# Kernel optimization log

Hardware: AMD Instinct MI355X
Metric: run time of the kernel (lower is better)

Reference implementation:

```python
import jax, jax.numpy as jnp
import numpy as np

N_NODES = 50000
N_EDGES = 500000
F_IN = 128
HID = 128
HEADS = 1
N_CLASSES = 5
NEG_SLOPE = 0.2   # PyG GATv2Conv default leaky_relu slope
BN_EPS = 1e-5


def setup_inputs() -> dict:
    key = jax.random.key(0)
    ks = jax.random.split(key, 16)
    d = {
        "x": jax.random.normal(ks[0], (N_NODES, F_IN), jnp.float32),
        "edge_index": jax.random.randint(ks[1], (2, N_EDGES), 0, N_NODES, jnp.int64),
        # GATv2Conv params (lin_l / lin_r with bias, attention vector, output bias)
        "Wl": jax.random.normal(ks[2], (F_IN, HEADS * HID), jnp.float32) * 0.05,
        "bl": jax.random.normal(ks[3], (HEADS * HID,), jnp.float32) * 0.05,
        "Wr": jax.random.normal(ks[4], (F_IN, HEADS * HID), jnp.float32) * 0.05,
        "br": jax.random.normal(ks[5], (HEADS * HID,), jnp.float32) * 0.05,
        "att": jax.random.normal(ks[6], (HEADS, HID), jnp.float32) * 0.05,
        "bias1": jax.random.normal(ks[7], (HID,), jnp.float32) * 0.05,
        # BatchNorm (eval mode: running stats + affine)
        "bn_gamma": jax.random.normal(ks[8], (HID,), jnp.float32) * 0.1 + 1.0,
        "bn_beta": jax.random.normal(ks[9], (HID,), jnp.float32) * 0.1,
        "bn_mean": jax.random.normal(ks[10], (HID,), jnp.float32) * 0.1,
        "bn_var": jax.random.uniform(ks[11], (HID,), jnp.float32, 0.5, 1.5),
        # classifier
        "Wc": jax.random.normal(ks[12], (HID, N_CLASSES), jnp.float32) * 0.05,
        "bc": jax.random.normal(ks[13], (N_CLASSES,), jnp.float32) * 0.05,
    }
    return d


def reference(x, edge_index, Wl, bl, Wr, br, att, bias1,
              bn_gamma, bn_beta, bn_mean, bn_var, Wc, bc):
    n = x.shape[0]
    heads, d = att.shape
    # PyG GATv2Conv default add_self_loops=True
    loops = jnp.arange(n, dtype=edge_index.dtype)
    src = jnp.concatenate([edge_index[0], loops])  # message source j
    dst = jnp.concatenate([edge_index[1], loops])  # aggregation target i

    xl = (x @ Wl + bl).reshape(n, heads, d)  # lin_l -> x_j side
    xr = (x @ Wr + br).reshape(n, heads, d)  # lin_r -> x_i side

    # per-edge GATv2 attention logits: a^T leaky_relu(x_j + x_i)
    e = jax.nn.leaky_relu(xl[src] + xr[dst], NEG_SLOPE)       # [E+N, H, D]
    logits = jnp.einsum('ehd,hd->eh', e, att)                 # [E+N, H]

    # segment softmax over incoming edges of each target node
    m = jax.ops.segment_max(logits, dst, num_segments=n)      # [N, H]
    a = jnp.exp(logits - m[dst])
    denom = jax.ops.segment_sum(a, dst, num_segments=n)
    a = a / denom[dst]                                        # [E+N, H]

    # weighted scatter-add of source features (dropout inactive at eval)
    out = jax.ops.segment_sum(xl[src] * a[:, :, None], dst, num_segments=n)  # [N,H,D]
    out = out.mean(axis=1) + bias1  # concat=False -> average heads, then bias

    # BatchNorm (eval: running stats)
    h = (out - bn_mean) * jax.lax.rsqrt(bn_var + BN_EPS) * bn_gamma + bn_beta

    # global_mean_pool with batch=None -> single graph
    g = h.mean(axis=0, keepdims=True)                         # [1, HID]
    return jax.nn.softmax(g @ Wc + bc, axis=1)                # [1, n_classes]
```

## Files before the change

### kernel.cpp

```cpp
#include <hip/hip_runtime.h>
#include <hip/hip_bf16.h>

typedef __attribute__((ext_vector_type(8))) short short8v;
typedef __attribute__((ext_vector_type(4))) float f32x4;
typedef __attribute__((ext_vector_type(2))) float v2f;

__device__ __forceinline__ unsigned short f2b(float f) {
    union { float f; unsigned int u; } v; v.f = f;
    unsigned int r = (v.u + 0x7fffu + ((v.u >> 16) & 1u)) >> 16;
    return (unsigned short)r;
}
__device__ __forceinline__ unsigned int pack2(float lo, float hi) {
    return (unsigned int)f2b(lo) | ((unsigned int)f2b(hi) << 16);
}
__device__ __forceinline__ void unpk_fp8x4(unsigned int u, float* o) {
    v2f lo = __builtin_amdgcn_cvt_pk_f32_fp8(u, false);
    v2f hi = __builtin_amdgcn_cvt_pk_f32_fp8(u, true);
    o[0] = lo[0]; o[1] = lo[1]; o[2] = hi[0]; o[3] = hi[1];
}

__global__ __launch_bounds__(256) void prep(
    const float* __restrict__ Wl, const float* __restrict__ bl,
    const float* __restrict__ Wr, const float* __restrict__ br,
    unsigned short* __restrict__ Whf, float* __restrict__ bh,
    float* __restrict__ zbuf, int nz)
{
    const int idx    = blockIdx.x * 256 + threadIdx.x;
    const int stride = gridDim.x * 256;

    for (int i = idx; i < 32768; i += stride) {
        int j   = i & 7;
        int l   = (i >> 3) & 63;
        int nfg = (i >> 9) & 15;
        int ks  = i >> 13;
        int k = ks * 32 + (l >> 4) * 8 + j;
        int c = nfg * 16 + (l & 15);
        float v = (c < 128) ? Wl[k * 128 + c] : Wr[k * 128 + (c - 128)];
        Whf[i] = f2b(v);
    }
    if (idx < 256) bh[idx] = (idx < 128) ? bl[idx] : br[idx - 128];
    for (int i = idx; i < nz; i += stride) zbuf[i] = 0.f;
}

#define GBM 64
__global__ __launch_bounds__(256) void gemm_mfma(
    const float* __restrict__ x, const unsigned short* __restrict__ Whf,
    const float* __restrict__ bh,
    unsigned char* __restrict__ XLq, unsigned char* __restrict__ XRq,
    int n)
{
    __shared__ unsigned short xs[GBM * 128];
    __shared__ unsigned char  lbuf[GBM][256];

    const int tid = threadIdx.x;
    const int w   = tid >> 6;
    const int l   = tid & 63;
    const int lr  = l & 15;
    const int lk  = l >> 4;

    short8v B[4][4];
    #pragma unroll
    for (int ks = 0; ks < 4; ++ks)
        #pragma unroll
        for (int nf = 0; nf < 4; ++nf)
            B[ks][nf] = *(const short8v*)&Whf[(((ks * 16 + (w * 4 + nf)) * 64 + l) << 3)];

    float biasv[4];
    #pragma unroll
    for (int nf = 0; nf < 4; ++nf) biasv[nf] = bh[w * 64 + nf * 16 + lr];

    const int sr  = tid >> 2;
    const int sc0 = (tid & 3) * 32;
    const int swz = (sr & 7) << 4;
    const int row0 = blockIdx.x * GBM;

    {
        const int grow = row0 + sr;
        if (grow < n) {
            const float4* src = (const float4*)&x[(size_t)grow * 128 + sc0];
            #pragma unroll
            for (int i = 0; i < 8; ++i) {
                float4 v = src[i];
                uint2 p; p.x = pack2(v.x, v.y); p.y = pack2(v.z, v.w);
                int byte = (sc0 + i * 4) * 2;
                *(uint2*)((char*)xs + sr * 256 + (byte ^ swz)) = p;
            }
        } else {
            uint2 p{0, 0};
            #pragma unroll
            for (int i = 0; i < 8; ++i) {
                int byte = (sc0 + i * 4) * 2;
                *(uint2*)((char*)xs + sr * 256 + (byte ^ swz)) = p;
            }
        }
    }
    __syncthreads();

    f32x4 acc[4][4];
    #pragma unroll
    for (int mf = 0; mf < 4; ++mf)
        #pragma unroll
        for (int nf = 0; nf < 4; ++nf)
            acc[mf][nf] = f32x4{0.f, 0.f, 0.f, 0.f};

    #pragma unroll
    for (int ks = 0; ks < 4; ++ks) {
        short8v A[4];
        #pragma unroll
        for (int mf = 0; mf < 4; ++mf) {
            int rr = mf * 16 + lr;
            int byte = (ks * 32 + lk * 8) * 2;
            A[mf] = *(short8v*)((char*)xs + rr * 256 + (byte ^ ((rr & 7) << 4)));
        }
        #pragma unroll
        for (int mf = 0; mf < 4; ++mf)
            #pragma unroll
            for (int nf = 0; nf < 4; ++nf)
                acc[mf][nf] = __builtin_amdgcn_mfma_f32_16x16x32_bf16(
                    A[mf], B[ks][nf], acc[mf][nf], 0, 0, 0);
    }

    #pragma unroll
    for (int mf = 0; mf < 4; ++mf) {
        #pragma unroll
        for (int nf = 0; nf < 4; ++nf) {
            const int ocol = w * 64 + nf * 16 + lr;
            #pragma unroll
            for (int j = 0; j < 4; ++j) {
                unsigned int u = __builtin_amdgcn_cvt_pk_fp8_f32(
                    acc[mf][nf][j] + biasv[nf], 0.f, 0u, false);
                lbuf[mf * 16 + lk * 4 + j][ocol] = (unsigned char)u;
            }
        }
    }
    __syncthreads();

    #pragma unroll
    for (int k = 0; k < 4; ++k) {
        const int ch  = k * 256 + tid;
        const int row = ch >> 4;
        const int seg = ch & 15;
        const int grow = row0 + row;
        if (grow < n) {
            uint4 v = *(const uint4*)&lbuf[row][seg * 16];
            if (seg < 8) *(uint4*)&XLq[(size_t)grow * 128 + seg * 16] = v;
            else         *(uint4*)&XRq[(size_t)grow * 128 + (seg - 8) * 16] = v;
        }
    }
}

__global__ __launch_bounds__(256) void edge_logits(
    const unsigned char* __restrict__ XLq, const unsigned char* __restrict__ XRq,
    const int* __restrict__ ei, const float* __restrict__ att,
    float* __restrict__ wbuf, float* __restrict__ denom,
    int nE, int nTot)
{
    const int e = (blockIdx.x * 256 + threadIdx.x) >> 3;
    if (e >= nTot) return;
    const int sub = threadIdx.x & 7;

    int src, dst;
    if (e < nE) { src = ei[e]; dst = ei[nE + e]; }
    else        { src = dst = e - nE; }

    uint4 ul = *(const uint4*)&XLq[(size_t)src * 128 + sub * 16];
    uint4 ur = *(const uint4*)&XRq[(size_t)dst * 128 + sub * 16];

    float fl[16], fr[16];
    unpk_fp8x4(ul.x, fl + 0); unpk_fp8x4(ul.y, fl + 4);
    unpk_fp8x4(ul.z, fl + 8); unpk_fp8x4(ul.w, fl + 12);
    unpk_fp8x4(ur.x, fr + 0); unpk_fp8x4(ur.y, fr + 4);
    unpk_fp8x4(ur.z, fr + 8); unpk_fp8x4(ur.w, fr + 12);

    const float4* ap = (const float4*)&att[sub * 16];
    float p = 0.f;
    #pragma unroll
    for (int q = 0; q < 4; ++q) {
        float4 a = ap[q];
        float s0 = fl[q*4+0] + fr[q*4+0];
        float s1 = fl[q*4+1] + fr[q*4+1];
        float s2 = fl[q*4+2] + fr[q*4+2];
        float s3 = fl[q*4+3] + fr[q*4+3];
        s0 = s0 > 0.f ? s0 : 0.2f*s0;  s1 = s1 > 0.f ? s1 : 0.2f*s1;
        s2 = s2 > 0.f ? s2 : 0.2f*s2;  s3 = s3 > 0.f ? s3 : 0.2f*s3;
        p += s0*a.x + s1*a.y + s2*a.z + s3*a.w;
    }

    #pragma unroll
    for (int m = 4; m >= 1; m >>= 1) p += __shfl_xor(p, m);

    if (sub == 0) {
        float wv = __expf(p);
        wbuf[e] = wv;
        atomicAdd(&denom[dst], wv);
    }
}

__global__ __launch_bounds__(256) void edge_coeff(
    const int* __restrict__ ei, const float* __restrict__ wbuf,
    const float* __restrict__ denom, float* __restrict__ csrc,
    int nE, int nTot)
{
    const int e = blockIdx.x * 256 + threadIdx.x;
    if (e >= nTot) return;
    int src, dst;
    if (e < nE) { src = ei[e]; dst = ei[nE + e]; }
    else        { src = dst = e - nE; }
    atomicAdd(&csrc[src], wbuf[e] / denom[dst]);
}

__global__ __launch_bounds__(256) void wsum(
    const unsigned char* __restrict__ XLq, const float* __restrict__ csrc,
    float* __restrict__ S, int n)
{
    const int sub = threadIdx.x & 7;
    const int grp = threadIdx.x >> 3;
    const int strd = gridDim.x * 32;

    float acc[16];
    #pragma unroll
    for (int k = 0; k < 16; ++k) acc[k] = 0.f;

    for (int j = blockIdx.x * 32 + grp; j < n; j += strd) {
        float cj = csrc[j];
        uint4 u = *(const uint4*)&XLq[(size_t)j * 128 + sub * 16];
        float f[16];
        unpk_fp8x4(u.x, f + 0); unpk_fp8x4(u.y, f + 4);
        unpk_fp8x4(u.z, f + 8); unpk_fp8x4(u.w, f + 12);
        #pragma unroll
        for (int k = 0; k < 16; ++k) acc[k] += cj * f[k];
    }

    __shared__ float sb[32][128];
    #pragma unroll
    for (int k = 0; k < 16; k += 4)
        *(float4*)&sb[grp][sub * 16 + k] = make_float4(acc[k], acc[k+1], acc[k+2], acc[k+3]);
    __syncthreads();

    if (threadIdx.x < 128) {
        float t = 0.f;
        #pragma unroll
        for (int g = 0; g < 32; ++g) t += sb[g][threadIdx.x];
        atomicAdd(&S[threadIdx.x], t);
    }
}

__global__ __launch_bounds__(128) void finalize(
    const float* __restrict__ S, const float* __restrict__ bias1,
    const float* __restrict__ gamma, const float* __restrict__ beta,
    const float* __restrict__ mean, const float* __restrict__ var,
    const float* __restrict__ Wc, const float* __restrict__ bc,
    float* __restrict__ out, int n)
{
    __shared__ float g[128];
    __shared__ float lg[5];
    const int t = threadIdx.x;

    float gv = (S[t] / (float)n + bias1[t] - mean[t])
             * rsqrtf(var[t] + 1e-5f) * gamma[t] + beta[t];
    g[t] = gv;
    __syncthreads();

    if (t < 5) {
        float acc = bc[t];
        #pragma unroll 16
        for (int d = 0; d < 128; ++d) acc += g[d] * Wc[d * 5 + t];
        lg[t] = acc;
    }
    __syncthreads();

    if (t == 0) {
        float m = lg[0];
        #pragma unroll
        for (int i = 1; i < 5; ++i) m = fmaxf(m, lg[i]);
        float ex[5]; float sum = 0.f;
        #pragma unroll
        for (int i = 0; i < 5; ++i) { ex[i] = expf(lg[i] - m); sum += ex[i]; }
        #pragma unroll
        for (int i = 0; i < 5; ++i) out[i] = ex[i] / sum;
    }
}

extern "C" void kernel_launch(void* const* d_in, const int* in_sizes, int n_in,
                              void* d_out, int out_size, void* d_ws, size_t ws_size,
                              hipStream_t stream)
{
    const float* x     = (const float*)d_in[0];
    const int*   ei    = (const int*)  d_in[1];
    const float* Wl    = (const float*)d_in[2];
    const float* bl    = (const float*)d_in[3];
    const float* Wr    = (const float*)d_in[4];
    const float* br    = (const float*)d_in[5];
    const float* att   = (const float*)d_in[6];
    const float* bias1 = (const float*)d_in[7];
    const float* gamma = (const float*)d_in[8];
    const float* beta  = (const float*)d_in[9];
    const float* mean  = (const float*)d_in[10];
    const float* var   = (const float*)d_in[11];
    const float* Wc    = (const float*)d_in[12];
    const float* bc    = (const float*)d_in[13];

    const int n    = in_sizes[0] / 128;
    const int nE   = in_sizes[1] / 2;
    const int nTot = nE + n;

    unsigned char* XLq = (unsigned char*)d_ws;
    unsigned char* XRq = XLq + (size_t)n * 128;
    unsigned short* Whf = (unsigned short*)(XRq + (size_t)n * 128);
    float* bh    = (float*)(Whf + 32768);
    float* wbuf  = bh + 256;
    float* denom = wbuf + nTot;
    float* csrc  = denom + n;
    float* S     = csrc + n;

    prep<<<512, 256, 0, stream>>>(Wl, bl, Wr, br, Whf, bh, denom, 2 * n + 128);

    const int ntiles = (n + GBM - 1) / GBM;
    gemm_mfma<<<ntiles, 256, 0, stream>>>(x, Whf, bh, XLq, XRq, n);

    edge_logits<<<(nTot * 8 + 255) / 256, 256, 0, stream>>>(
        XLq, XRq, ei, att, wbuf, denom, nE, nTot);

    edge_coeff<<<(nTot + 255) / 256, 256, 0, stream>>>(ei, wbuf, denom, csrc, nE, nTot);

    wsum<<<512, 256, 0, stream>>>(XLq, csrc, S, n);

    finalize<<<1, 128, 0, stream>>>(S, bias1, gamma, beta, mean, var, Wc, bc,
                                    (float*)d_out, n);
}
```

Measured before the change: 106.2 us.

## Fuse prep into GEMM and finalize into wsum via last-block counter

Drops the separate prep kernel: each GEMM block now loads the fp32 Wl/Wr columns it needs directly, converts them to bf16 fragments, and zeroes its slice of the accumulator buffers. The finalize kernel is folded into wsum through an atomic block counter, so the last block to finish computes the BatchNorm, classifier and softmax. This saves two kernel launches and their inter-kernel gaps. In exchange every GEMM block does strided uncoalesced weight loads, and correctness relies on the counter being zeroed before wsum_fin and on thread fences.

```diff
diff --git a/kernel.cpp b/kernel.cpp
--- a/kernel.cpp
+++ b/kernel.cpp
@@ -19,55 +19,45 @@
     o[0] = lo[0]; o[1] = lo[1]; o[2] = hi[0]; o[3] = hi[1];
 }
 
-__global__ __launch_bounds__(256) void prep(
+#define GBM 64
+__global__ __launch_bounds__(256) void gemm_mfma(
+    const float* __restrict__ x,
     const float* __restrict__ Wl, const float* __restrict__ bl,
     const float* __restrict__ Wr, const float* __restrict__ br,
-    unsigned short* __restrict__ Whf, float* __restrict__ bh,
-    float* __restrict__ zbuf, int nz)
-{
-    const int idx    = blockIdx.x * 256 + threadIdx.x;
-    const int stride = gridDim.x * 256;
-
-    for (int i = idx; i < 32768; i += stride) {
-        int j   = i & 7;
-        int l   = (i >> 3) & 63;
-        int nfg = (i >> 9) & 15;
-        int ks  = i >> 13;
-        int k = ks * 32 + (l >> 4) * 8 + j;
-        int c = nfg * 16 + (l & 15);
-        float v = (c < 128) ? Wl[k * 128 + c] : Wr[k * 128 + (c - 128)];
-        Whf[i] = f2b(v);
-    }
-    if (idx < 256) bh[idx] = (idx < 128) ? bl[idx] : br[idx - 128];
-    for (int i = idx; i < nz; i += stride) zbuf[i] = 0.f;
-}
-
-#define GBM 64
-__global__ __launch_bounds__(256) void gemm_mfma(
-    const float* __restrict__ x, const unsigned short* __restrict__ Whf,
-    const float* __restrict__ bh,
     unsigned char* __restrict__ XLq, unsigned char* __restrict__ XRq,
-    int n)
+    int n, float* __restrict__ zbuf, int nz)
 {
     __shared__ unsigned short xs[GBM * 128];
     __shared__ unsigned char  lbuf[GBM][256];
 
     const int tid = threadIdx.x;
+
+    {
+        const int zi = blockIdx.x * 256 + tid;
+        if (zi < nz) zbuf[zi] = 0.f;
+    }
+
     const int w   = tid >> 6;
     const int l   = tid & 63;
     const int lr  = l & 15;
     const int lk  = l >> 4;
 
     short8v B[4][4];
-    #pragma unroll
-    for (int ks = 0; ks < 4; ++ks)
-        #pragma unroll
-        for (int nf = 0; nf < 4; ++nf)
-            B[ks][nf] = *(const short8v*)&Whf[(((ks * 16 + (w * 4 + nf)) * 64 + l) << 3)];
-
     float biasv[4];
     #pragma unroll
-    for (int nf = 0; nf < 4; ++nf) biasv[nf] = bh[w * 64 + nf * 16 + lr];
+    for (int nf = 0; nf < 4; ++nf) {
+        const int col = w * 64 + nf * 16 + lr;
+        const float* Wp = (col < 128) ? (Wl + col) : (Wr + (col - 128));
+        biasv[nf] = (col < 128) ? bl[col] : br[col - 128];
+        #pragma unroll
+        for (int ks = 0; ks < 4; ++ks) {
+            short8v b;
+            #pragma unroll
+            for (int j = 0; j < 8; ++j)
+                b[j] = (short)f2b(Wp[(ks * 32 + lk * 8 + j) * 128]);
+            B[ks][nf] = b;
+        }
+    }
 
     const int sr  = tid >> 2;
     const int sc0 = (tid & 3) * 32;
@@ -209,9 +199,14 @@
     atomicAdd(&csrc[src], wbuf[e] / denom[dst]);
 }
 
-__global__ __launch_bounds__(256) void wsum(
+__global__ __launch_bounds__(256) void wsum_fin(
     const unsigned char* __restrict__ XLq, const float* __restrict__ csrc,
-    float* __restrict__ S, int n)
+    float* __restrict__ S, unsigned int* __restrict__ counter, int n,
+    const float* __restrict__ bias1,
+    const float* __restrict__ gamma, const float* __restrict__ beta,
+    const float* __restrict__ mean, const float* __restrict__ var,
+    const float* __restrict__ Wc, const float* __restrict__ bc,
+    float* __restrict__ out)
 {
     const int sub = threadIdx.x & 7;
     const int grp = threadIdx.x >> 3;
@@ -243,32 +238,32 @@
         for (int g = 0; g < 32; ++g) t += sb[g][threadIdx.x];
         atomicAdd(&S[threadIdx.x], t);
     }
-}
-
-__global__ __launch_bounds__(128) void finalize(
-    const float* __restrict__ S, const float* __restrict__ bias1,
-    const float* __restrict__ gamma, const float* __restrict__ beta,
-    const float* __restrict__ mean, const float* __restrict__ var,
-    const float* __restrict__ Wc, const float* __restrict__ bc,
-    float* __restrict__ out, int n)
-{
-    __shared__ float g[128];
+
+    __threadfence();
+    __shared__ unsigned int isLast;
+    if (threadIdx.x == 0) {
+        unsigned int old = atomicAdd(counter, 1u);
+        isLast = (old == (unsigned int)gridDim.x - 1u) ? 1u : 0u;
+    }
+    __syncthreads();
+    if (!isLast) return;
+
+    __shared__ float gbuf[128];
     __shared__ float lg[5];
     const int t = threadIdx.x;
-
-    float gv = (S[t] / (float)n + bias1[t] - mean[t])
-             * rsqrtf(var[t] + 1e-5f) * gamma[t] + beta[t];
-    g[t] = gv;
-    __syncthreads();
-
+    if (t < 128) {
+        float sv = atomicAdd(&S[t], 0.f);
+        gbuf[t] = (sv / (float)n + bias1[t] - mean[t])
+                * rsqrtf(var[t] + 1e-5f) * gamma[t] + beta[t];
+    }
+    __syncthreads();
     if (t < 5) {
-        float acc = bc[t];
+        float a = bc[t];
         #pragma unroll 16
-        for (int d = 0; d < 128; ++d) acc += g[d] * Wc[d * 5 + t];
-        lg[t] = acc;
-    }
-    __syncthreads();
-
+        for (int d = 0; d < 128; ++d) a += gbuf[d] * Wc[d * 5 + t];
+        lg[t] = a;
+    }
+    __syncthreads();
     if (t == 0) {
         float m = lg[0];
         #pragma unroll
@@ -306,25 +301,23 @@
 
     unsigned char* XLq = (unsigned char*)d_ws;
     unsigned char* XRq = XLq + (size_t)n * 128;
-    unsigned short* Whf = (unsigned short*)(XRq + (size_t)n * 128);
-    float* bh    = (float*)(Whf + 32768);
-    float* wbuf  = bh + 256;
+    float* wbuf  = (float*)(XRq + (size_t)n * 128);
     float* denom = wbuf + nTot;
     float* csrc  = denom + n;
     float* S     = csrc + n;
-
-    prep<<<512, 256, 0, stream>>>(Wl, bl, Wr, br, Whf, bh, denom, 2 * n + 128);
+    unsigned int* counter = (unsigned int*)(S + 128);
+    const int nz = 2 * n + 128 + 1;
 
     const int ntiles = (n + GBM - 1) / GBM;
-    gemm_mfma<<<ntiles, 256, 0, stream>>>(x, Whf, bh, XLq, XRq, n);
+    gemm_mfma<<<ntiles, 256, 0, stream>>>(x, Wl, bl, Wr, br, XLq, XRq, n,
+                                          denom, nz);
 
     edge_logits<<<(nTot * 8 + 255) / 256, 256, 0, stream>>>(
         XLq, XRq, ei, att, wbuf, denom, nE, nTot);
 
     edge_coeff<<<(nTot + 255) / 256, 256, 0, stream>>>(ei, wbuf, denom, csrc, nE, nTot);
 
-    wsum<<<512, 256, 0, stream>>>(XLq, csrc, S, n);
-
-    finalize<<<1, 128, 0, stream>>>(S, bias1, gamma, beta, mean, var, Wc, bc,
-                                    (float*)d_out, n);
-}
+    wsum_fin<<<512, 256, 0, stream>>>(XLq, csrc, S, counter, n,
+                                      bias1, gamma, beta, mean, var, Wc, bc,
+                                      (float*)d_out);
+}
```

Measured after the change: 132.1 us. 24.3% more time.
